# Optimization experiments

Measured on AMD Instinct MI355X. Metric: run time of the kernel, lower is better.

Reference implementation:

```python
import jax, jax.numpy as jnp
import numpy as np

NUM_BINS = 256

def setup_inputs() -> dict:
    key = jax.random.key(0)
    k1, k2 = jax.random.split(key)
    B, C, H, W = 32, 3, 512, 512
    # images in [-1, 1], matching the torch module's denorm x*0.5+0.5
    imgs = jax.random.uniform(k1, (B, C, H, W), dtype=jnp.float32) * 2.0 - 1.0
    target_hist = jax.random.uniform(k2, (B, NUM_BINS), dtype=jnp.float32)
    return {"generated_img_batch": imgs, "target_hist_batch": target_hist}


def _batch_histograms(images, num_bins):
    # images: [B, C, H, W] in [-1, 1]
    B = images.shape[0]
    denorm = images * 0.5 + 0.5                       # [0, 1]
    idx = (denorm * (num_bins - 1)).astype(jnp.int32)  # [B, C, H, W]
    idx = idx.reshape(B, -1)                           # [B, C*H*W]
    rows = jnp.arange(B, dtype=jnp.int32)[:, None]
    hist = jnp.zeros((B, num_bins), dtype=jnp.float32)
    hist = hist.at[rows, idx].add(1.0)
    return hist


def reference(generated_img_batch, target_hist_batch):
    eps = 1e-8
    gen_hist = _batch_histograms(generated_img_batch, NUM_BINS)
    gen_p = gen_hist / (gen_hist.sum(axis=1, keepdims=True) + eps)
    tgt_p = target_hist_batch / (target_hist_batch.sum(axis=1, keepdims=True) + eps)
    gen_cdf = jnp.cumsum(gen_p, axis=1)
    tgt_cdf = jnp.cumsum(tgt_p, axis=1)
    return jnp.mean(jnp.abs(gen_cdf - tgt_cdf))
```

## Files before the change

kernel.cpp:

```cpp
#include <hip/hip_runtime.h>

#define NUM_BINS 256
#define BATCH 32
#define CHW (3 * 512 * 512)
#define N4 (CHW / 4)
#define BLOCKS_PER_BATCH 192

__global__ __launch_bounds__(256) void hist_kernel(
    const float* __restrict__ img, unsigned int* __restrict__ hist) {
  __shared__ unsigned int lh[4][NUM_BINS];
  const int tid  = threadIdx.x;
  const int wave = tid >> 6;
  const int b    = blockIdx.y;

  for (int i = tid; i < 4 * NUM_BINS; i += 256)
    ((unsigned int*)lh)[i] = 0u;
  __syncthreads();

  const float4* src = (const float4*)(img + (size_t)b * CHW);
  const int stride = BLOCKS_PER_BATCH * 256;
  for (int i = blockIdx.x * 256 + tid; i < N4; i += stride) {
    float4 v = src[i];
    int i0 = (int)((v.x * 0.5f + 0.5f) * 255.0f);
    int i1 = (int)((v.y * 0.5f + 0.5f) * 255.0f);
    int i2 = (int)((v.z * 0.5f + 0.5f) * 255.0f);
    int i3 = (int)((v.w * 0.5f + 0.5f) * 255.0f);
    i0 = min(max(i0, 0), NUM_BINS - 1);
    i1 = min(max(i1, 0), NUM_BINS - 1);
    i2 = min(max(i2, 0), NUM_BINS - 1);
    i3 = min(max(i3, 0), NUM_BINS - 1);
    atomicAdd(&lh[wave][i0], 1u);
    atomicAdd(&lh[wave][i1], 1u);
    atomicAdd(&lh[wave][i2], 1u);
    atomicAdd(&lh[wave][i3], 1u);
  }
  __syncthreads();

  if (tid < NUM_BINS) {
    unsigned int s = lh[0][tid] + lh[1][tid] + lh[2][tid] + lh[3][tid];
    if (s) atomicAdd(&hist[b * NUM_BINS + tid], s);
  }
}

__global__ __launch_bounds__(256) void loss_kernel(
    const unsigned int* __restrict__ hist, const float* __restrict__ tgt,
    float* __restrict__ partial) {
  __shared__ float s[NUM_BINS];
  const int b = blockIdx.x, tid = threadIdx.x;

  float g = (float)hist[b * NUM_BINS + tid];
  float t = tgt[b * NUM_BINS + tid];

  s[tid] = g; __syncthreads();
  for (int off = 128; off > 0; off >>= 1) {
    if (tid < off) s[tid] += s[tid + off];
    __syncthreads();
  }
  float sg = s[0]; __syncthreads();

  s[tid] = t; __syncthreads();
  for (int off = 128; off > 0; off >>= 1) {
    if (tid < off) s[tid] += s[tid + off];
    __syncthreads();
  }
  float st = s[0]; __syncthreads();

  float v = g / (sg + 1e-8f) - t / (st + 1e-8f);

  s[tid] = v; __syncthreads();
  for (int off = 1; off < NUM_BINS; off <<= 1) {
    float a = (tid >= off) ? s[tid - off] : 0.0f;
    __syncthreads();
    v += a;
    s[tid] = v;
    __syncthreads();
  }

  s[tid] = fabsf(v); __syncthreads();
  for (int off = 128; off > 0; off >>= 1) {
    if (tid < off) s[tid] += s[tid + off];
    __syncthreads();
  }
  if (tid == 0) partial[b] = s[0];
}

__global__ __launch_bounds__(64) void final_kernel(
    const float* __restrict__ partial, float* __restrict__ out) {
  const int tid = threadIdx.x;
  float v = (tid < BATCH) ? partial[tid] : 0.0f;
  for (int off = 32; off > 0; off >>= 1) v += __shfl_down(v, off);
  if (tid == 0) out[0] = v / (float)(BATCH * NUM_BINS);
}

extern "C" void kernel_launch(void* const* d_in, const int* in_sizes, int n_in,
                              void* d_out, int out_size, void* d_ws, size_t ws_size,
                              hipStream_t stream) {
  const float* img = (const float*)d_in[0];
  const float* tgt = (const float*)d_in[1];
  float* out = (float*)d_out;

  unsigned int* hist = (unsigned int*)d_ws;
  float* partial = (float*)((char*)d_ws + BATCH * NUM_BINS * 4);

  hipMemsetAsync(hist, 0, BATCH * NUM_BINS * sizeof(unsigned int), stream);

  dim3 hgrid(BLOCKS_PER_BATCH, BATCH, 1);
  hist_kernel<<<hgrid, 256, 0, stream>>>(img, hist);
  loss_kernel<<<BATCH, 256, 0, stream>>>(hist, tgt, partial);
  final_kernel<<<1, 64, 0, stream>>>(partial, out);
}
```

Measured before the change: 151.4 us.

## Drop memset and final kernel, write per-block histograms, fuse final reduction

The histogram kernel now writes per-block partial histograms to a workspace buffer instead of using global atomics. This removes the memset and cuts blocks per batch from 192 to 64, using a fixed-trip loop unrolled by 4. The loss kernel sums the 64 partials per bin, uses wave shuffles instead of shared-memory tree reductions and scans, and has the last block (found via an atomic counter) compute the final mean. This removes two launches, but fewer blocks may reduce memory-level parallelism on the 100MB streaming read.

Result: no change. 149.5 us (-1.3%).

```diff
diff --git a/kernel.cpp b/kernel.cpp
--- a/kernel.cpp
+++ b/kernel.cpp
@@ -4,22 +4,29 @@
 #define BATCH 32
 #define CHW (3 * 512 * 512)
 #define N4 (CHW / 4)
-#define BLOCKS_PER_BATCH 192
+#define BPB 64
+
+#define GH_ELEMS (BATCH * BPB * NUM_BINS)
 
 __global__ __launch_bounds__(256) void hist_kernel(
-    const float* __restrict__ img, unsigned int* __restrict__ hist) {
+    const float* __restrict__ img, unsigned int* __restrict__ gh,
+    unsigned int* __restrict__ counter) {
   __shared__ unsigned int lh[4][NUM_BINS];
   const int tid  = threadIdx.x;
   const int wave = tid >> 6;
+  const int blk  = blockIdx.x;
   const int b    = blockIdx.y;
+
+  if (blk == 0 && b == 0 && tid == 0) *counter = 0u;
 
   for (int i = tid; i < 4 * NUM_BINS; i += 256)
     ((unsigned int*)lh)[i] = 0u;
   __syncthreads();
 
   const float4* src = (const float4*)(img + (size_t)b * CHW);
-  const int stride = BLOCKS_PER_BATCH * 256;
-  for (int i = blockIdx.x * 256 + tid; i < N4; i += stride) {
+  int i = blk * 256 + tid;
+#pragma unroll 4
+  for (int it = 0; it < N4 / (BPB * 256); ++it, i += BPB * 256) {
     float4 v = src[i];
     int i0 = (int)((v.x * 0.5f + 0.5f) * 255.0f);
     int i1 = (int)((v.y * 0.5f + 0.5f) * 255.0f);
@@ -36,60 +43,73 @@
   }
   __syncthreads();
 
-  if (tid < NUM_BINS) {
-    unsigned int s = lh[0][tid] + lh[1][tid] + lh[2][tid] + lh[3][tid];
-    if (s) atomicAdd(&hist[b * NUM_BINS + tid], s);
-  }
+  unsigned int s = lh[0][tid] + lh[1][tid] + lh[2][tid] + lh[3][tid];
+  gh[((size_t)b * BPB + blk) * NUM_BINS + tid] = s;
 }
 
 __global__ __launch_bounds__(256) void loss_kernel(
-    const unsigned int* __restrict__ hist, const float* __restrict__ tgt,
-    float* __restrict__ partial) {
-  __shared__ float s[NUM_BINS];
+    const unsigned int* __restrict__ gh, const float* __restrict__ tgt,
+    float* __restrict__ partial, unsigned int* __restrict__ counter,
+    float* __restrict__ out) {
+  __shared__ float2 wsum[4];
+  __shared__ float wtot[4];
+  __shared__ float wabs[4];
+  __shared__ int last_flag;
   const int b = blockIdx.x, tid = threadIdx.x;
+  const int lane = tid & 63, wave = tid >> 6;
 
-  float g = (float)hist[b * NUM_BINS + tid];
+  float g = 0.0f;
+  const unsigned int* gb = gh + (size_t)b * BPB * NUM_BINS + tid;
+#pragma unroll 8
+  for (int k = 0; k < BPB; ++k) g += (float)gb[k * NUM_BINS];
   float t = tgt[b * NUM_BINS + tid];
 
-  s[tid] = g; __syncthreads();
-  for (int off = 128; off > 0; off >>= 1) {
-    if (tid < off) s[tid] += s[tid + off];
-    __syncthreads();
+  float sg = g, st = t;
+#pragma unroll
+  for (int off = 32; off > 0; off >>= 1) {
+    sg += __shfl_down(sg, off);
+    st += __shfl_down(st, off);
   }
-  float sg = s[0]; __syncthreads();
+  if (lane == 0) wsum[wave] = make_float2(sg, st);
+  __syncthreads();
+  float sgT = wsum[0].x + wsum[1].x + wsum[2].x + wsum[3].x;
+  float stT = wsum[0].y + wsum[1].y + wsum[2].y + wsum[3].y;
 
-  s[tid] = t; __syncthreads();
-  for (int off = 128; off > 0; off >>= 1) {
-    if (tid < off) s[tid] += s[tid + off];
-    __syncthreads();
+  float v = g / (sgT + 1e-8f) - t / (stT + 1e-8f);
+
+  float sv = v;
+#pragma unroll
+  for (int off = 1; off < 64; off <<= 1) {
+    float n = __shfl_up(sv, off);
+    if (lane >= off) sv += n;
   }
-  float st = s[0]; __syncthreads();
+  if (lane == 63) wtot[wave] = sv;
+  __syncthreads();
+  float prefix = 0.0f;
+  for (int w = 0; w < wave; ++w) prefix += wtot[w];
+  sv += prefix;
 
-  float v = g / (sg + 1e-8f) - t / (st + 1e-8f);
+  float a = fabsf(sv);
+#pragma unroll
+  for (int off = 32; off > 0; off >>= 1) a += __shfl_down(a, off);
+  if (lane == 0) wabs[wave] = a;
+  __syncthreads();
 
-  s[tid] = v; __syncthreads();
-  for (int off = 1; off < NUM_BINS; off <<= 1) {
-    float a = (tid >= off) ? s[tid - off] : 0.0f;
-    __syncthreads();
-    v += a;
-    s[tid] = v;
-    __syncthreads();
+  if (tid == 0) {
+    float tot = wabs[0] + wabs[1] + wabs[2] + wabs[3];
+    atomicExch(&partial[b], tot);
+    __threadfence();
+    unsigned int old = atomicAdd(counter, 1u);
+    last_flag = (old == BATCH - 1) ? 1 : 0;
   }
+  __syncthreads();
 
-  s[tid] = fabsf(v); __syncthreads();
-  for (int off = 128; off > 0; off >>= 1) {
-    if (tid < off) s[tid] += s[tid + off];
-    __syncthreads();
+  if (last_flag && wave == 0) {
+    float pv = (lane < BATCH) ? atomicAdd(&partial[lane], 0.0f) : 0.0f;
+#pragma unroll
+    for (int off = 32; off > 0; off >>= 1) pv += __shfl_down(pv, off);
+    if (lane == 0) out[0] = pv / (float)(BATCH * NUM_BINS);
   }
-  if (tid == 0) partial[b] = s[0];
-}
-
-__global__ __launch_bounds__(64) void final_kernel(
-    const float* __restrict__ partial, float* __restrict__ out) {
-  const int tid = threadIdx.x;
-  float v = (tid < BATCH) ? partial[tid] : 0.0f;
-  for (int off = 32; off > 0; off >>= 1) v += __shfl_down(v, off);
-  if (tid == 0) out[0] = v / (float)(BATCH * NUM_BINS);
 }
 
 extern "C" void kernel_launch(void* const* d_in, const int* in_sizes, int n_in,
@@ -99,13 +119,11 @@
   const float* tgt = (const float*)d_in[1];
   float* out = (float*)d_out;
 
-  unsigned int* hist = (unsigned int*)d_ws;
-  float* partial = (float*)((char*)d_ws + BATCH * NUM_BINS * 4);
+  unsigned int* gh = (unsigned int*)d_ws;
+  float* partial = (float*)((char*)d_ws + GH_ELEMS * sizeof(unsigned int));
+  unsigned int* counter = (unsigned int*)(partial + BATCH);
 
-  hipMemsetAsync(hist, 0, BATCH * NUM_BINS * sizeof(unsigned int), stream);
-
-  dim3 hgrid(BLOCKS_PER_BATCH, BATCH, 1);
-  hist_kernel<<<hgrid, 256, 0, stream>>>(img, hist);
-  loss_kernel<<<BATCH, 256, 0, stream>>>(hist, tgt, partial);
-  final_kernel<<<1, 64, 0, stream>>>(partial, out);
+  dim3 hgrid(BPB, BATCH, 1);
+  hist_kernel<<<hgrid, 256, 0, stream>>>(img, gh, counter);
+  loss_kernel<<<BATCH, 256, 0, stream>>>(gh, tgt, partial, counter, out);
 }
```
